# Kernel optimization log

Hardware: AMD Instinct MI355X
Metric: run time of the kernel (lower is better)

Reference implementation:

```python
import jax, jax.numpy as jnp
import numpy as np

IN_SIZE = 1024
OUT_SIZE = 4096
LOGN = 12          # ceil(log2(max(in,out)))
N = 1 << LOGN      # 4096
BATCH = 8192


def setup_inputs() -> dict:
    key = jax.random.key(0)
    k1, k2, k3 = jax.random.split(key, 3)
    # kaiming_uniform on [2*logN, N]: fan_in = N, bound = sqrt(6/fan_in)
    bound = float(np.sqrt(6.0 / N))
    learned_params = jax.random.uniform(k1, (2 * LOGN, N), minval=-bound, maxval=bound, dtype=jnp.float32)
    inp = jax.random.normal(k2, (BATCH, IN_SIZE), dtype=jnp.float32)
    # np.random.permutation(N)[:out_size]
    out_row_indices = jax.random.permutation(k3, N)[:OUT_SIZE].astype(jnp.int32)
    return {"input": inp, "learned_params": learned_params, "out_row_indices": out_row_indices}


def reference(input, learned_params, out_row_indices):
    # Build B = prod_i (diag(p[2i]) + P_i @ diag(p[2i+1])), P_i[j, j^2^i] = 1.
    # (P_i @ diag(d) @ B)[j, :] = d[j^2^i] * B[j^2^i, :], so each layer is a
    # row-scale + xor-permuted row-scale of B (same math as the dense matmul chain).
    B = jnp.eye(N, dtype=input.dtype)
    for i in range(LOGN):
        perm = jnp.arange(N) ^ (1 << i)  # static per layer
        B = learned_params[2 * i][:, None] * B + learned_params[2 * i + 1][perm][:, None] * B[perm]
    layer_matrix = B[out_row_indices, :IN_SIZE]   # [out_size, in_size]
    return input @ layer_matrix.T                  # [batch, out_size]
```

## Files before the change

### kernel.cpp

```cpp
#include <hip/hip_runtime.h>


typedef float f4 __attribute__((ext_vector_type(4)));
typedef float f2 __attribute__((ext_vector_type(2)));
typedef int   i4 __attribute__((ext_vector_type(4)));

__device__ __forceinline__ int swz(int e) {
    return e ^ (((e >> 5) & 3) << 2);
}

template<int CTRL>
__device__ __forceinline__ float dppx(float x) {
    int xi = __builtin_bit_cast(int, x);
    int r  = __builtin_amdgcn_update_dpp(xi, xi, CTRL, 0xF, 0xF, true);
    return __builtin_bit_cast(float, r);
}

__global__ void __launch_bounds__(256) bfly_prep(
    const float* __restrict__ lp, const int* __restrict__ orow,
    float* __restrict__ scale, int* __restrict__ src2)
{
    int j = blockIdx.x * 256 + threadIdx.x;
    if (j >= 4096) return;
    int r = orow[j];
    int c = r & 1023;
    int u = r & 2047;
    const float* A10 = lp + 20 * 4096;
    const float* B10 = lp + 21 * 4096;
    const float* A11 = lp + 22 * 4096;
    const float* B11 = lp + 23 * 4096;
    float f11 = (r & 2048) ? B11[u] : A11[u];
    float f10 = (r & 1024) ? B10[c] : A10[c];
    scale[j] = f11 * f10;
    src2[j] = c ^ (((c >> 4) & 7) << 1);
}

__global__ void __launch_bounds__(256, 4) bfly_main(
    const float* __restrict__ inp, const float* __restrict__ lp,
    const float* __restrict__ scale, const int* __restrict__ src2,
    float* __restrict__ out)
{
    __shared__ __align__(16) float cf[10 * 1024];
    const int t = threadIdx.x;
    const int wave = t >> 6, lane = t & 63;

    #pragma unroll
    for (int q = 0; q < 10; ++q) {
        const f4 v = *reinterpret_cast<const f4*>(lp + (size_t)(10 + q) * 4096 + t * 4);
        *reinterpret_cast<f4*>(&cf[q * 1024 + swz(t * 4)]) = v;
    }

    const int sBase = blockIdx.x * 8 + wave * 2;
    float x[2][16];
    #pragma unroll
    for (int m = 0; m < 2; ++m) {
        const f4* p = reinterpret_cast<const f4*>(inp + (size_t)(sBase + m) * 1024 + lane * 16);
        #pragma unroll
        for (int c = 0; c < 4; ++c) {
            f4 v = p[c];
            x[m][4*c+0] = v.x; x[m][4*c+1] = v.y; x[m][4*c+2] = v.z; x[m][4*c+3] = v.w;
        }
    }

    __syncthreads();

    #pragma unroll
    for (int i = 0; i < 2; ++i) {
        const f4* A = reinterpret_cast<const f4*>(lp + (size_t)(2*i)   * 4096 + lane * 16);
        const f4* B = reinterpret_cast<const f4*>(lp + (size_t)(2*i+1) * 4096 + lane * 16);
        #pragma unroll
        for (int c = 0; c < 4; ++c) {
            f4 va = A[c], vb = B[c];
            #pragma unroll
            for (int m = 0; m < 2; ++m) {
                float* xm = x[m];
                if (i == 0) {
                    float lo0 = xm[4*c+0], hi0 = xm[4*c+1];
                    xm[4*c+0] = va[0] * lo0 + vb[1] * hi0;
                    xm[4*c+1] = va[1] * hi0 + vb[0] * lo0;
                    float lo1 = xm[4*c+2], hi1 = xm[4*c+3];
                    xm[4*c+2] = va[2] * lo1 + vb[3] * hi1;
                    xm[4*c+3] = va[3] * hi1 + vb[2] * lo1;
                } else {
                    float lo0 = xm[4*c+0], hi0 = xm[4*c+2];
                    xm[4*c+0] = va[0] * lo0 + vb[2] * hi0;
                    xm[4*c+2] = va[2] * hi0 + vb[0] * lo0;
                    float lo1 = xm[4*c+1], hi1 = xm[4*c+3];
                    xm[4*c+1] = va[1] * lo1 + vb[3] * hi1;
                    xm[4*c+3] = va[3] * hi1 + vb[1] * lo1;
                }
            }
        }
    }

    #pragma unroll
    for (int i = 2; i < 4; ++i) {
        const f4* A = reinterpret_cast<const f4*>(lp + (size_t)(2*i)   * 4096 + lane * 16);
        const f4* B = reinterpret_cast<const f4*>(lp + (size_t)(2*i+1) * 4096 + lane * 16);
        #pragma unroll
        for (int g = 0; g < 2; ++g) {
            const int q0 = (i == 2) ? 2 * g : g;
            const int q1 = (i == 2) ? q0 + 1 : q0 + 2;
            f4 va0 = A[q0], va1 = A[q1], vb0 = B[q0], vb1 = B[q1];
            #pragma unroll
            for (int m = 0; m < 2; ++m) {
                float* xm = x[m];
                #pragma unroll
                for (int e = 0; e < 4; ++e) {
                    float lo = xm[4*q0+e], hi = xm[4*q1+e];
                    xm[4*q0+e] = va0[e] * lo + vb1[e] * hi;
                    xm[4*q1+e] = va1[e] * hi + vb0[e] * lo;
                }
            }
        }
    }

    {
        const f4* A = reinterpret_cast<const f4*>(lp + (size_t)8 * 4096 + lane * 16);
        const f4* B = reinterpret_cast<const f4*>(lp + (size_t)9 * 4096 + (lane ^ 1) * 16);
        #pragma unroll
        for (int c = 0; c < 4; ++c) {
            f4 va = A[c], vb = B[c];
            #pragma unroll
            for (int m = 0; m < 2; ++m) {
                #pragma unroll
                for (int e = 0; e < 4; ++e) {
                    float v = x[m][4*c+e];
                    x[m][4*c+e] = va[e] * v + vb[e] * dppx<0xB1>(v);
                }
            }
        }
    }

    #pragma unroll
    for (int i = 5; i < 10; ++i) {
        const int d = 1 << (i - 4);
        const float* arow = &cf[(size_t)(i - 5) * 2048];
        const float* brow = arow + 1024;
        #pragma unroll
        for (int c = 0; c < 4; ++c) {
            f4 va = *reinterpret_cast<const f4*>(&arow[swz(lane * 16 + 4 * c)]);
            f4 vb = *reinterpret_cast<const f4*>(&brow[swz((lane ^ d) * 16 + 4 * c)]);
            #pragma unroll
            for (int m = 0; m < 2; ++m) {
                #pragma unroll
                for (int e = 0; e < 4; ++e) {
                    float v = x[m][4*c+e];
                    float xp = (d == 2) ? dppx<0x4E>(v)
                             : (d == 8) ? dppx<0x128>(v)
                             :            __shfl_xor(v, d, 64);
                    x[m][4*c+e] = va[e] * v + vb[e] * xp;
                }
            }
        }
    }

    __syncthreads();

    float* zz = &cf[(size_t)wave * 2048];
    const int km0 = (lane & 7) << 1;

    #pragma unroll
    for (int k = 0; k < 16; k += 2) {
        int pi = lane * 16 + (k ^ km0);
        f4 v = { x[0][k], x[1][k], x[0][k+1], x[1][k+1] };
        *reinterpret_cast<f4*>(&zz[2 * pi]) = v;
    }

    const i4* srv = reinterpret_cast<const i4*>(src2);
    const f4* scv = reinterpret_cast<const f4*>(scale);
    f4* o0 = reinterpret_cast<f4*>(out + (size_t)sBase * 4096);
    f4* o1 = reinterpret_cast<f4*>(out + (size_t)(sBase + 1) * 4096);

    i4 si = srv[lane];
    f4 sc = scv[lane];
    #pragma unroll
    for (int it = 0; it < 16; ++it) {
        i4 si_c = si;
        f4 sc_c = sc;
        if (it + 1 < 16) {
            si = srv[(it + 1) * 64 + lane];
            sc = scv[(it + 1) * 64 + lane];
        }
        int j4 = it * 64 + lane;
        f2 vx = *reinterpret_cast<const f2*>(&zz[2 * si_c.x]);
        f2 vy = *reinterpret_cast<const f2*>(&zz[2 * si_c.y]);
        f2 vz = *reinterpret_cast<const f2*>(&zz[2 * si_c.z]);
        f2 vw = *reinterpret_cast<const f2*>(&zz[2 * si_c.w]);
        f4 r0 = { sc_c.x * vx.x, sc_c.y * vy.x, sc_c.z * vz.x, sc_c.w * vw.x };
        f4 r1 = { sc_c.x * vx.y, sc_c.y * vy.y, sc_c.z * vz.y, sc_c.w * vw.y };
        o0[j4] = r0;
        o1[j4] = r1;
    }
}

extern "C" void kernel_launch(void* const* d_in, const int* in_sizes, int n_in,
                              void* d_out, int out_size, void* d_ws, size_t ws_size,
                              hipStream_t stream) {
    const float* inp  = (const float*)d_in[0];
    const float* lp   = (const float*)d_in[1];
    const int*   orow = (const int*)d_in[2];
    float* out = (float*)d_out;

    float* scale = (float*)d_ws;
    int*   src2  = (int*)((char*)d_ws + 4096 * 4);

    bfly_prep<<<16, 256, 0, stream>>>(lp, orow, scale, src2);
    bfly_main<<<1024, 256, 0, stream>>>(inp, lp, scale, src2, out);
}
```

Before: 45.53 us.

## Stage all butterfly coefficients in LDS with 512-thread blocks and separate scratch

Blocks grow to 512 threads (16 rows each) and the kernel now stages all 20 coefficient rows of layers 0-9 in LDS instead of 10. Layers 0-4 previously read their coefficients straight from global memory through per-lane vector loads; they now read swizzled LDS. Each wave's transpose scratch sits in its own LDS region, so the second __syncthreads is gone. LDS per block rises to about 144KB, which limits occupancy to one block per CU and may serialise latency hiding.

```diff
diff --git a/kernel.cpp b/kernel.cpp
--- a/kernel.cpp
+++ b/kernel.cpp
@@ -35,22 +35,24 @@
     src2[j] = c ^ (((c >> 4) & 7) << 1);
 }
 
-__global__ void __launch_bounds__(256, 4) bfly_main(
+__global__ void __launch_bounds__(512, 2) bfly_main(
     const float* __restrict__ inp, const float* __restrict__ lp,
     const float* __restrict__ scale, const int* __restrict__ src2,
     float* __restrict__ out)
 {
-    __shared__ __align__(16) float cf[10 * 1024];
+    __shared__ __align__(16) float cf[20 * 1024 + 8 * 2048];
     const int t = threadIdx.x;
     const int wave = t >> 6, lane = t & 63;
 
     #pragma unroll
-    for (int q = 0; q < 10; ++q) {
-        const f4 v = *reinterpret_cast<const f4*>(lp + (size_t)(10 + q) * 4096 + t * 4);
-        *reinterpret_cast<f4*>(&cf[q * 1024 + swz(t * 4)]) = v;
-    }
-
-    const int sBase = blockIdx.x * 8 + wave * 2;
+    for (int step = 0; step < 10; ++step) {
+        const int q = 2 * step + (t >> 8);
+        const int e = (t & 255) * 4;
+        const f4 v = *reinterpret_cast<const f4*>(lp + (size_t)q * 4096 + e);
+        *reinterpret_cast<f4*>(&cf[q * 1024 + swz(e)]) = v;
+    }
+
+    const int sBase = blockIdx.x * 16 + wave * 2;
     float x[2][16];
     #pragma unroll
     for (int m = 0; m < 2; ++m) {
@@ -66,11 +68,12 @@
 
     #pragma unroll
     for (int i = 0; i < 2; ++i) {
-        const f4* A = reinterpret_cast<const f4*>(lp + (size_t)(2*i)   * 4096 + lane * 16);
-        const f4* B = reinterpret_cast<const f4*>(lp + (size_t)(2*i+1) * 4096 + lane * 16);
-        #pragma unroll
-        for (int c = 0; c < 4; ++c) {
-            f4 va = A[c], vb = B[c];
+        const float* arow = &cf[(size_t)(2*i)     * 1024];
+        const float* brow = &cf[(size_t)(2*i + 1) * 1024];
+        #pragma unroll
+        for (int c = 0; c < 4; ++c) {
+            f4 va = *reinterpret_cast<const f4*>(&arow[swz(lane * 16 + 4 * c)]);
+            f4 vb = *reinterpret_cast<const f4*>(&brow[swz(lane * 16 + 4 * c)]);
             #pragma unroll
             for (int m = 0; m < 2; ++m) {
                 float* xm = x[m];
@@ -95,13 +98,16 @@
 
     #pragma unroll
     for (int i = 2; i < 4; ++i) {
-        const f4* A = reinterpret_cast<const f4*>(lp + (size_t)(2*i)   * 4096 + lane * 16);
-        const f4* B = reinterpret_cast<const f4*>(lp + (size_t)(2*i+1) * 4096 + lane * 16);
+        const float* arow = &cf[(size_t)(2*i)     * 1024];
+        const float* brow = &cf[(size_t)(2*i + 1) * 1024];
         #pragma unroll
         for (int g = 0; g < 2; ++g) {
             const int q0 = (i == 2) ? 2 * g : g;
             const int q1 = (i == 2) ? q0 + 1 : q0 + 2;
-            f4 va0 = A[q0], va1 = A[q1], vb0 = B[q0], vb1 = B[q1];
+            f4 va0 = *reinterpret_cast<const f4*>(&arow[swz(lane * 16 + 4 * q0)]);
+            f4 va1 = *reinterpret_cast<const f4*>(&arow[swz(lane * 16 + 4 * q1)]);
+            f4 vb0 = *reinterpret_cast<const f4*>(&brow[swz(lane * 16 + 4 * q0)]);
+            f4 vb1 = *reinterpret_cast<const f4*>(&brow[swz(lane * 16 + 4 * q1)]);
             #pragma unroll
             for (int m = 0; m < 2; ++m) {
                 float* xm = x[m];
@@ -116,11 +122,12 @@
     }
 
     {
-        const f4* A = reinterpret_cast<const f4*>(lp + (size_t)8 * 4096 + lane * 16);
-        const f4* B = reinterpret_cast<const f4*>(lp + (size_t)9 * 4096 + (lane ^ 1) * 16);
-        #pragma unroll
-        for (int c = 0; c < 4; ++c) {
-            f4 va = A[c], vb = B[c];
+        const float* arow = &cf[(size_t)8 * 1024];
+        const float* brow = &cf[(size_t)9 * 1024];
+        #pragma unroll
+        for (int c = 0; c < 4; ++c) {
+            f4 va = *reinterpret_cast<const f4*>(&arow[swz(lane * 16 + 4 * c)]);
+            f4 vb = *reinterpret_cast<const f4*>(&brow[swz((lane ^ 1) * 16 + 4 * c)]);
             #pragma unroll
             for (int m = 0; m < 2; ++m) {
                 #pragma unroll
@@ -135,8 +142,8 @@
     #pragma unroll
     for (int i = 5; i < 10; ++i) {
         const int d = 1 << (i - 4);
-        const float* arow = &cf[(size_t)(i - 5) * 2048];
-        const float* brow = arow + 1024;
+        const float* arow = &cf[(size_t)(2*i)     * 1024];
+        const float* brow = &cf[(size_t)(2*i + 1) * 1024];
         #pragma unroll
         for (int c = 0; c < 4; ++c) {
             f4 va = *reinterpret_cast<const f4*>(&arow[swz(lane * 16 + 4 * c)]);
@@ -155,11 +162,8 @@
         }
     }
 
-    __syncthreads();
-
-    float* zz = &cf[(size_t)wave * 2048];
+    float* zz = &cf[20 * 1024 + (size_t)wave * 2048];
     const int km0 = (lane & 7) << 1;
-
     #pragma unroll
     for (int k = 0; k < 16; k += 2) {
         int pi = lane * 16 + (k ^ km0);
@@ -206,5 +210,5 @@
     int*   src2  = (int*)((char*)d_ws + 4096 * 4);
 
     bfly_prep<<<16, 256, 0, stream>>>(lp, orow, scale, src2);
-    bfly_main<<<1024, 256, 0, stream>>>(inp, lp, scale, src2, out);
-}
+    bfly_main<<<512, 512, 0, stream>>>(inp, lp, scale, src2, out);
+}
```

New measurement: 42.47 us. -6.7%, faster.
